# Optimization experiments

Measured on AMD Instinct MI355X. Metric: run time of the kernel, lower is better.

Reference implementation:

```python
import jax, jax.numpy as jnp
import numpy as np

N, E, NB = 50000, 100000, 6          # nodes, directed messages, max neighbors
NF, BF, H, DEPTH = 98, 6, 256, 6     # node feat, bond feat, hidden, depth
EF = NF + BF                          # edge_fdim: hmess = [fnode[src], bond_feats]


def setup_inputs() -> dict:
    key = jax.random.key(0)
    ks = jax.random.split(key, 12)
    s = lambda fan: np.float32(1.0 / np.sqrt(fan))
    return {
        "fnode": jax.random.normal(ks[0], (N, NF), jnp.float32),
        "fmess_idx": jax.random.randint(ks[1], (E, 2), 0, N),
        "fmess_feat": jax.random.normal(ks[2], (E, BF), jnp.float32),
        "agraph": jax.random.randint(ks[3], (N, NB), 0, E),
        "bgraph": jax.random.randint(ks[4], (E, NB), 0, E),
        "Wz": jax.random.normal(ks[5], (3, EF + H, H), jnp.float32) * s(EF + H),
        "bz": jnp.zeros((3, H), jnp.float32),
        "Wr": jax.random.normal(ks[6], (3, EF, H), jnp.float32) * s(EF),
        "Ur": jax.random.normal(ks[7], (3, H, H), jnp.float32) * s(H),
        "bur": jnp.zeros((3, H), jnp.float32),
        "Wh": jax.random.normal(ks[8], (3, EF + H, H), jnp.float32) * s(EF + H),
        "bh": jnp.zeros((3, H), jnp.float32),
        "Wo": jax.random.normal(ks[9], (3, NF + H, H), jnp.float32) * s(NF + H),
        "bo": jnp.zeros((3, H), jnp.float32),
    }


def _mpn(hnode, hmess, agraph, bgraph, Wz, bz, Wr, Ur, bur, Wh, bh, Wo, bo):
    # One MPNLayer: depth-unrolled message GRU over bgraph, then node readout via agraph.
    e_mask = jnp.ones((hmess.shape[0], 1), hmess.dtype).at[0, 0].set(0.0)  # msg 0 = padding
    r1 = hmess @ Wr  # W_r(fmess), loop-invariant  [E,H]

    def step(h, _):
        h_nei = h[bgraph]                                    # [E,NB,H] gather inbound msgs
        sum_h = h_nei.sum(axis=1)
        z = jax.nn.sigmoid(jnp.concatenate([hmess, sum_h], axis=1) @ Wz + bz)
        r = jax.nn.sigmoid(r1[:, None, :] + h_nei @ Ur + bur)  # [E,NB,H]
        sum_gh = (r * h_nei).sum(axis=1)
        pre_h = jnp.tanh(jnp.concatenate([hmess, sum_gh], axis=1) @ Wh + bh)
        return ((1.0 - z) * sum_h + z * pre_h) * e_mask, None

    h0 = jnp.zeros((hmess.shape[0], bz.shape[0]), hmess.dtype)
    h, _ = jax.lax.scan(step, h0, None, length=DEPTH)
    nei = h[agraph].sum(axis=1)                              # [N,H]
    node_h = jax.nn.relu(jnp.concatenate([hnode, nei], axis=1) @ Wo + bo)
    n_mask = jnp.ones((hnode.shape[0], 1), hnode.dtype).at[0, 0].set(0.0)  # node 0 = padding
    return node_h * n_mask


def reference(fnode, fmess_idx, fmess_feat, agraph, bgraph,
              Wz, bz, Wr, Ur, bur, Wh, bh, Wo, bo):
    # embed_graph: gather source-node features, concat with bond features
    hmess = jnp.concatenate([fnode[fmess_idx[:, 0]], fmess_feat], axis=1)  # [E,EF]
    run = jax.vmap(lambda a, b, c, d, e, f, g, hh, i: _mpn(
        fnode, hmess, agraph, bgraph, a, b, c, d, e, f, g, hh, i))
    qkv = run(Wz, bz, Wr, Ur, bur, Wh, bh, Wo, bo)           # [3,N,H]: Q/K/V encoders batched
    return (qkv[0], qkv[1], qkv[2])
```

## Files before the change

kernel.cpp:

```cpp
#include <hip/hip_runtime.h>


#define NE 100000
#define NEP 100032
#define NN 50000

typedef unsigned short u16;
typedef short short8 __attribute__((ext_vector_type(8)));
typedef float f32x4 __attribute__((ext_vector_type(4)));
typedef unsigned short u16x4 __attribute__((ext_vector_type(4)));

__device__ __forceinline__ float b2f(u16 u) {
  union { unsigned int i; float f; } v; v.i = ((unsigned int)u) << 16; return v.f;
}
__device__ __forceinline__ u16 f2b(float f) {
  union { float f; unsigned int i; } v; v.f = f;
  unsigned int b = v.i;
  b += 0x7FFFu + ((b >> 16) & 1u);
  return (u16)(b >> 16);
}
__device__ __forceinline__ unsigned cvtpk(float lo, float hi) {
  unsigned r;
  asm("v_cvt_pk_bf16_f32 %0, %1, %2" : "=v"(r) : "v"(lo), "v"(hi));
  return r;
}
__device__ __forceinline__ int swzB(int Q) { return Q ^ ((Q >> 4) & 7); }
__device__ __forceinline__ float sigm(float x) { return 1.0f / (1.0f + __expf(-x)); }
__device__ __forceinline__ float tanh_f(float x) { return 2.0f / (1.0f + __expf(-2.0f * x)) - 1.0f; }
__device__ __forceinline__ f32x4 mfma16(short8 a, short8 b, f32x4 c) {
  return __builtin_amdgcn_mfma_f32_16x16x32_bf16(a, b, c, 0, 0, 0);
}

__global__ void pack_wpre(const float* __restrict__ Wr, const float* __restrict__ Wz,
                          const float* __restrict__ Wh, u16* __restrict__ dst) {
  const int g = blockIdx.y;
  const int p = blockIdx.x * 256 + threadIdx.x;
  const int j = p & 7, l = (p >> 3) & 63, q = p >> 9;
  const int nb = q % 48, s = q / 48;
  const int k = 32 * s + 8 * (l >> 4) + j;
  const int n = 16 * nb + (l & 15);
  float v = 0.f;
  if (k < 104) {
    if (n < 256)      v = Wr[((size_t)g * 104 + k) * 256 + n];
    else if (n < 512) v = Wz[((size_t)g * 360 + k) * 256 + (n - 256)];
    else              v = Wh[((size_t)g * 360 + k) * 256 + (n - 512)];
  }
  dst[(size_t)g * 98304 + p] = f2b(v);
}

__global__ void pack_wgate(const float* __restrict__ Wz, const float* __restrict__ Wh,
                           u16* __restrict__ dst) {
  const int g = blockIdx.y;
  const int p = blockIdx.x * 256 + threadIdx.x;
  const int j = p & 7, l = (p >> 3) & 63, q = p >> 9;
  const int nb = q % 32, s = q / 32;
  const int k = 32 * s + 8 * (l >> 4) + j;
  const int n = 16 * nb + (l & 15);
  float v = (n < 256) ? Wz[((size_t)g * 360 + 104 + k) * 256 + n]
                      : Wh[((size_t)g * 360 + 104 + k) * 256 + (n - 256)];
  dst[(size_t)g * 131072 + p] = f2b(v);
}

__global__ void pack_ur(const float* __restrict__ Ur, u16* __restrict__ dst) {
  const int g = blockIdx.y;
  const int p = blockIdx.x * 256 + threadIdx.x;
  const int j = p & 7, l = (p >> 3) & 63, q = p >> 9;
  const int nb = q % 16, s = q / 16;
  const int k = 32 * s + 8 * (l >> 4) + j;
  const int n = 16 * nb + (l & 15);
  dst[(size_t)g * 65536 + p] = f2b(Ur[((size_t)g * 256 + k) * 256 + n]);
}

__global__ void pack_wo(const float* __restrict__ Wo, u16* __restrict__ dst) {
  const int g = blockIdx.y;
  const int p = blockIdx.x * 256 + threadIdx.x;
  const int j = p & 7, l = (p >> 3) & 63, q = p >> 9;
  const int nb = q % 16, s = q / 16;
  const int k = 32 * s + 8 * (l >> 4) + j;
  const int n = 16 * nb + (l & 15);
  float v = 0.f;
  if (k < 98)        v = Wo[((size_t)g * 354 + k) * 256 + n];
  else if (k >= 128) v = Wo[((size_t)g * 354 + (k - 30)) * 256 + n];
  dst[(size_t)g * 98304 + p] = f2b(v);
}

__global__ void embed_hmess_f(const float* __restrict__ fnode, const int* __restrict__ fmess_idx,
                              const float* __restrict__ fmess_feat, u16* __restrict__ hmF) {
  const int e = blockIdx.x * 2 + (threadIdx.x >> 7);
  const int c = threadIdx.x & 127;
  const int src = fmess_idx[e * 2];
  float v = 0.f;
  if (c < 98)       v = fnode[(size_t)src * 98 + c];
  else if (c < 104) v = fmess_feat[(size_t)e * 6 + (c - 98)];
  hmF[(size_t)(e >> 4) * 2048 + ((c >> 5) * 64 + (e & 15) + 16 * ((c >> 3) & 3)) * 8 + (c & 7)] = f2b(v);
}

__global__ void embed_fnode(const float* __restrict__ fnode, u16* __restrict__ fnp) {
  const int n = blockIdx.x * 2 + (threadIdx.x >> 7);
  const int c = threadIdx.x & 127;
  float v = (c < 98) ? fnode[(size_t)n * 98 + c] : 0.f;
  fnp[(size_t)n * 128 + c] = f2b(v);
}

__global__ __launch_bounds__(256)
void pre_gemm_t(const u16* __restrict__ hmF, const u16* __restrict__ Wpre,
                const float* __restrict__ bur, const float* __restrict__ bz,
                const float* __restrict__ bh, u16* __restrict__ r1b,
                u16* __restrict__ zpF, u16* __restrict__ hpF) {
  const int tid = threadIdx.x, wave = tid >> 6, lane = tid & 63;
  const int row0 = lane & 15, kq = lane >> 4;
  const int e0 = blockIdx.x * 32;
  const int cchunk = blockIdx.y;
  f32x4 acc[2][4];
#pragma unroll
  for (int i = 0; i < 2; ++i)
#pragma unroll
    for (int n = 0; n < 4; ++n) { acc[i][n][0]=0.f; acc[i][n][1]=0.f; acc[i][n][2]=0.f; acc[i][n][3]=0.f; }
#pragma unroll
  for (int kc = 0; kc < 4; ++kc) {
    short8 bf[2];
#pragma unroll
    for (int ef = 0; ef < 2; ++ef)
      bf[ef] = *(const short8*)(hmF + (size_t)((e0 >> 4) + ef) * 2048 + (size_t)(kc * 64 + lane) * 8);
#pragma unroll
    for (int nf = 0; nf < 4; ++nf) {
      const int nb = cchunk * 16 + wave * 4 + nf;
      short8 wf = *(const short8*)(Wpre + ((size_t)(kc * 48 + nb) * 64 + lane) * 8);
      acc[0][nf] = mfma16(wf, bf[0], acc[0][nf]);
      acc[1][nf] = mfma16(wf, bf[1], acc[1][nf]);
    }
  }
  const float* bias = (cchunk == 0) ? bur : (cchunk == 1 ? bz : bh);
  u16* dstF = (cchunk == 1) ? zpF : hpF;
#pragma unroll
  for (int ef = 0; ef < 2; ++ef)
#pragma unroll
    for (int nf = 0; nf < 4; ++nf) {
      const int n256 = wave * 64 + nf * 16 + kq * 4;
      const int e = e0 + ef * 16 + row0;
      u16x4 o;
#pragma unroll
      for (int v = 0; v < 4; ++v) o[v] = f2b(acc[ef][nf][v] + bias[n256 + v]);
      if (cchunk == 0) {
        *(u16x4*)(r1b + (size_t)e * 256 + n256) = o;
      } else {
        *(u16x4*)(dstF + ((size_t)((e0 >> 4) + ef) * 16 + (wave * 4 + nf)) * 256 + lane * 4) = o;
      }
    }
}

__global__ __launch_bounds__(512, 4)
void mpn_fused(const u16* __restrict__ HBin, u16* __restrict__ HBout,
               const u16* __restrict__ r1b, const int* __restrict__ bgraph,
               const u16* __restrict__ zpF, const u16* __restrict__ hpF,
               const u16* __restrict__ Wgate, const u16* __restrict__ Urp) {
  __shared__ __align__(16) u16 sF[32768];
  const int tid = threadIdx.x;
  const int wn = tid >> 6, lane = tid & 63;
  const int row0 = lane & 15, kq = lane >> 4;
  const int e0 = blockIdx.x * 64;

  {
    const int c0 = 4 * lane;
    const int Bc = (c0 >> 5) * 64 + 16 * ((c0 >> 3) & 3);
    const int sub = c0 & 7;
#pragma unroll 2
    for (int rr = 0; rr < 8; ++rr) {
      const int r = wn * 8 + rr;
      const int e = e0 + r;
      float sh[4] = {0.f, 0.f, 0.f, 0.f}, sg[4] = {0.f, 0.f, 0.f, 0.f};
      if (e < NE) {
        const u16x4 r1v = *(const u16x4*)(r1b + (size_t)e * 256 + c0);
        int idx[6];
#pragma unroll
        for (int k = 0; k < 6; ++k) idx[k] = bgraph[e * 6 + k];
        u16x4 hv[6], huv[6];
#pragma unroll
        for (int k = 0; k < 6; ++k) {
          const u16* rowp = HBin + (size_t)idx[k] * 512;
          hv[k]  = *(const u16x4*)(rowp + c0);
          huv[k] = *(const u16x4*)(rowp + 256 + c0);
        }
#pragma unroll
        for (int k = 0; k < 6; ++k)
#pragma unroll
          for (int j = 0; j < 4; ++j) {
            const float h  = b2f(hv[k][j]);
            const float rg = sigm(b2f(r1v[j]) + b2f(huv[k][j]));
            sh[j] += h;
            sg[j] += rg * h;
          }
      }
      const int Q = (r >> 4) * 512 + Bc + (r & 15);
      const int ao = swzB(Q) * 8 + sub;
      union { unsigned w[2]; u16x4 q; } p0, p1;
      p0.w[0] = cvtpk(sh[0], sh[1]); p0.w[1] = cvtpk(sh[2], sh[3]);
      p1.w[0] = cvtpk(sg[0], sg[1]); p1.w[1] = cvtpk(sg[2], sg[3]);
      *(u16x4*)(sF + ao) = p0.q;
      *(u16x4*)(sF + 16384 + ao) = p1.q;
    }
  }
  __syncthreads();

  f32x4 aZ[2][4], aH[2][4];
#pragma unroll
  for (int nf = 0; nf < 2; ++nf)
#pragma unroll
    for (int ef = 0; ef < 4; ++ef) {
      aZ[nf][ef][0]=0.f; aZ[nf][ef][1]=0.f; aZ[nf][ef][2]=0.f; aZ[nf][ef][3]=0.f;
      aH[nf][ef][0]=0.f; aH[nf][ef][1]=0.f; aH[nf][ef][2]=0.f; aH[nf][ef][3]=0.f;
    }
#pragma unroll
  for (int kc = 0; kc < 8; ++kc) {
    short8 wz0 = *(const short8*)(Wgate + ((size_t)(kc * 32 + wn * 2 + 0) * 64 + lane) * 8);
    short8 wz1 = *(const short8*)(Wgate + ((size_t)(kc * 32 + wn * 2 + 1) * 64 + lane) * 8);
    short8 wh0 = *(const short8*)(Wgate + ((size_t)(kc * 32 + 16 + wn * 2 + 0) * 64 + lane) * 8);
    short8 wh1 = *(const short8*)(Wgate + ((size_t)(kc * 32 + 16 + wn * 2 + 1) * 64 + lane) * 8);
#pragma unroll
    for (int ef = 0; ef < 4; ++ef) {
      const int ar = swzB(ef * 512 + kc * 64 + lane) * 8;
      short8 bsh = *(const short8*)(sF + ar);
      short8 bsg = *(const short8*)(sF + 16384 + ar);
      aZ[0][ef] = mfma16(wz0, bsh, aZ[0][ef]);
      aZ[1][ef] = mfma16(wz1, bsh, aZ[1][ef]);
      aH[0][ef] = mfma16(wh0, bsg, aH[0][ef]);
      aH[1][ef] = mfma16(wh1, bsg, aH[1][ef]);
    }
  }

  u16x4 hq[2][4];
#pragma unroll
  for (int nf = 0; nf < 2; ++nf) {
    const int lp = row0 + 16 * (nf * 2 + (kq >> 1));
    const int jo = 4 * (kq & 1);
    const int nc = wn * 2 + nf;
#pragma unroll
    for (int ef = 0; ef < 4; ++ef) {
      const int ev = (e0 + ef * 16) < NE;
      const int e  = e0 + ef * 16 + row0;
      const int as = swzB(ef * 512 + wn * 64 + lp) * 8 + jo;
      const u16x4 shv = *(const u16x4*)(sF + as);
      const size_t tb = ((size_t)((e0 >> 4) + ef) * 16 + nc) * 256 + lane * 4;
      const u16x4 zp4 = *(const u16x4*)(zpF + tb);
      const u16x4 hp4 = *(const u16x4*)(hpF + tb);
      float hf[4];
#pragma unroll
      for (int v = 0; v < 4; ++v) {
        const float z  = sigm(b2f(zp4[v]) + aZ[nf][ef][v]);
        const float ph = tanh_f(b2f(hp4[v]) + aH[nf][ef][v]);
        float h = (1.0f - z) * b2f(shv[v]) + z * ph;
        if (e == 0 || !ev) h = 0.f;
        hf[v] = h;
      }
      union { unsigned w[2]; u16x4 q; } pk;
      pk.w[0] = cvtpk(hf[0], hf[1]);
      pk.w[1] = cvtpk(hf[2], hf[3]);
      hq[nf][ef] = pk.q;
    }
  }
  __syncthreads();

#pragma unroll
  for (int nf = 0; nf < 2; ++nf) {
    const int lp = row0 + 16 * (nf * 2 + (kq >> 1));
    const int jo = 4 * (kq & 1);
#pragma unroll
    for (int ef = 0; ef < 4; ++ef) {
      const int as = swzB(ef * 512 + wn * 64 + lp) * 8 + jo;
      *(u16x4*)(sF + 16384 + as) = hq[nf][ef];
    }
  }
  __syncthreads();

  f32x4 aU[2][4];
#pragma unroll
  for (int nf = 0; nf < 2; ++nf)
#pragma unroll
    for (int ef = 0; ef < 4; ++ef) { aU[nf][ef][0]=0.f; aU[nf][ef][1]=0.f; aU[nf][ef][2]=0.f; aU[nf][ef][3]=0.f; }
#pragma unroll
  for (int kc = 0; kc < 8; ++kc) {
    short8 u0 = *(const short8*)(Urp + ((size_t)(kc * 16 + wn * 2 + 0) * 64 + lane) * 8);
    short8 u1 = *(const short8*)(Urp + ((size_t)(kc * 16 + wn * 2 + 1) * 64 + lane) * 8);
#pragma unroll
    for (int ef = 0; ef < 4; ++ef) {
      const int ar = swzB(ef * 512 + kc * 64 + lane) * 8;
      short8 hb = *(const short8*)(sF + 16384 + ar);
      aU[0][ef] = mfma16(u0, hb, aU[0][ef]);
      aU[1][ef] = mfma16(u1, hb, aU[1][ef]);
    }
  }

  {
    const int r = tid >> 3;
    const int e = e0 + r;
    if (e < NE) {
#pragma unroll
      for (int it = 0; it < 4; ++it) {
        const int c = (tid & 7) * 8 + it * 64;
        const int Qn = (r >> 4) * 512 + (c >> 5) * 64 + (r & 15) + 16 * ((c >> 3) & 3);
        const short8 val = *(const short8*)(sF + 16384 + swzB(Qn) * 8);
        *(short8*)(HBout + (size_t)e * 512 + c) = val;
      }
    }
  }
#pragma unroll
  for (int nf = 0; nf < 2; ++nf) {
    const int lp = row0 + 16 * (nf * 2 + (kq >> 1));
    const int jo = 4 * (kq & 1);
#pragma unroll
    for (int ef = 0; ef < 4; ++ef) {
      const int as = swzB(ef * 512 + wn * 64 + lp) * 8 + jo;
      union { unsigned w[2]; u16x4 q; } pk;
      pk.w[0] = cvtpk(aU[nf][ef][0], aU[nf][ef][1]);
      pk.w[1] = cvtpk(aU[nf][ef][2], aU[nf][ef][3]);
      *(u16x4*)(sF + as) = pk.q;
    }
  }
  __syncthreads();

  {
    const int r = tid >> 3;
    const int e = e0 + r;
    if (e < NE) {
#pragma unroll
      for (int it = 0; it < 4; ++it) {
        const int c = (tid & 7) * 8 + it * 64;
        const int Qn = (r >> 4) * 512 + (c >> 5) * 64 + (r & 15) + 16 * ((c >> 3) & 3);
        const short8 val = *(const short8*)(sF + swzB(Qn) * 8);
        *(short8*)(HBout + (size_t)e * 512 + 256 + c) = val;
      }
    }
  }
}

__global__ __launch_bounds__(512, 4)
void step0(u16* __restrict__ HB, const u16* __restrict__ zpF, const u16* __restrict__ hpF,
           const u16* __restrict__ Urp) {
  __shared__ __align__(16) u16 sHn[16384];
  const int tid = threadIdx.x;
  const int wn = tid >> 6, lane = tid & 63;
  const int row0 = lane & 15, kq = lane >> 4;
  const int e0 = blockIdx.x * 64;

#pragma unroll
  for (int nf = 0; nf < 2; ++nf) {
    const int lp = row0 + 16 * (nf * 2 + (kq >> 1));
    const int jo = 4 * (kq & 1);
    const int nc = wn * 2 + nf;
#pragma unroll
    for (int ef = 0; ef < 4; ++ef) {
      const int ev = (e0 + ef * 16) < NE;
      const int e  = e0 + ef * 16 + row0;
      const size_t tb = ((size_t)((e0 >> 4) + ef) * 16 + nc) * 256 + lane * 4;
      const u16x4 zp4 = *(const u16x4*)(zpF + tb);
      const u16x4 hp4 = *(const u16x4*)(hpF + tb);
      u16x4 hq;
#pragma unroll
      for (int v = 0; v < 4; ++v) {
        float hf = sigm(b2f(zp4[v])) * tanh_f(b2f(hp4[v]));
        if (e == 0 || !ev) hf = 0.f;
        hq[v] = f2b(hf);
      }
      *(u16x4*)(sHn + (size_t)ef * 4096 + (size_t)(wn * 64 + lp) * 8 + jo) = hq;
    }
  }
  __syncthreads();

  f32x4 aU[2][4];
#pragma unroll
  for (int nf = 0; nf < 2; ++nf)
#pragma unroll
    for (int ef = 0; ef < 4; ++ef) { aU[nf][ef][0]=0.f; aU[nf][ef][1]=0.f; aU[nf][ef][2]=0.f; aU[nf][ef][3]=0.f; }
#pragma unroll
  for (int kc = 0; kc < 8; ++kc) {
    short8 u0 = *(const short8*)(Urp + ((size_t)(kc * 16 + wn * 2 + 0) * 64 + lane) * 8);
    short8 u1 = *(const short8*)(Urp + ((size_t)(kc * 16 + wn * 2 + 1) * 64 + lane) * 8);
#pragma unroll
    for (int ef = 0; ef < 4; ++ef) {
      short8 hb = *(const short8*)(sHn + (size_t)ef * 4096 + (size_t)(kc * 64 + lane) * 8);
      aU[0][ef] = mfma16(u0, hb, aU[0][ef]);
      aU[1][ef] = mfma16(u1, hb, aU[1][ef]);
    }
  }
  {
    const int r = tid >> 3;
    const int e = e0 + r;
    if (e < NE) {
#pragma unroll
      for (int it = 0; it < 4; ++it) {
        const int c = (tid & 7) * 8 + it * 64;
        const short8 val = *(const short8*)(sHn + (size_t)(r >> 4) * 4096 +
                           (size_t)(((c >> 5) * 64 + (r & 15) + 16 * ((c >> 3) & 3)) * 8));
        *(short8*)(HB + (size_t)e * 512 + c) = val;
      }
    }
  }
  __syncthreads();
#pragma unroll
  for (int nf = 0; nf < 2; ++nf) {
    const int lp = row0 + 16 * (nf * 2 + (kq >> 1));
    const int jo = 4 * (kq & 1);
#pragma unroll
    for (int ef = 0; ef < 4; ++ef) {
      u16x4 uq;
#pragma unroll
      for (int v = 0; v < 4; ++v) uq[v] = f2b(aU[nf][ef][v]);
      *(u16x4*)(sHn + (size_t)ef * 4096 + (size_t)(wn * 64 + lp) * 8 + jo) = uq;
    }
  }
  __syncthreads();
  {
    const int r = tid >> 3;
    const int e = e0 + r;
    if (e < NE) {
#pragma unroll
      for (int it = 0; it < 4; ++it) {
        const int c = (tid & 7) * 8 + it * 64;
        const short8 val = *(const short8*)(sHn + (size_t)(r >> 4) * 4096 +
                           (size_t)(((c >> 5) * 64 + (r & 15) + 16 * ((c >> 3) & 3)) * 8));
        *(short8*)(HB + (size_t)e * 512 + 256 + c) = val;
      }
    }
  }
}

__global__ __launch_bounds__(256)
void readout(const u16* __restrict__ HB, const u16* __restrict__ fnp,
             const int* __restrict__ agraph, const u16* __restrict__ Wop,
             const float* __restrict__ bo, float* __restrict__ out) {
  __shared__ __align__(16) u16 sN[32][264];
  const int tid = threadIdx.x, wave = tid >> 6, lane = tid & 63;
  const int n0 = blockIdx.x * 32;
  const int row0 = lane & 15, kq = lane >> 4;

#pragma unroll 2
  for (int rr = 0; rr < 8; ++rr) {
    const int r = wave * 8 + rr;
    const int n = n0 + r;
    float s4[4] = {0.f, 0.f, 0.f, 0.f};
    if (n < NN) {
#pragma unroll
      for (int k = 0; k < 6; ++k) {
        const int idx = agraph[n * 6 + k];
        const u16x4 hv = *(const u16x4*)(HB + (size_t)idx * 512 + 4 * lane);
#pragma unroll
        for (int j = 0; j < 4; ++j) s4[j] += b2f(hv[j]);
      }
    }
#pragma unroll
    for (int j = 0; j < 4; ++j) sN[r][4 * lane + j] = f2b(s4[j]);
  }
  __syncthreads();

  f32x4 acc[2][4];
#pragma unroll
  for (int i = 0; i < 2; ++i)
#pragma unroll
    for (int n = 0; n < 4; ++n) { acc[i][n][0]=0.f; acc[i][n][1]=0.f; acc[i][n][2]=0.f; acc[i][n][3]=0.f; }
  const int ra = min(n0 + row0, NN - 1);
  const int rb = min(n0 + 16 + row0, NN - 1);
#pragma unroll
  for (int s = 0; s < 12; ++s) {
    short8 a0, a1;
    if (s < 4) {
      a0 = *(const short8*)(fnp + (size_t)ra * 128 + s * 32 + kq * 8);
      a1 = *(const short8*)(fnp + (size_t)rb * 128 + s * 32 + kq * 8);
    } else {
      a0 = *(const short8*)&sN[row0][(s - 4) * 32 + kq * 8];
      a1 = *(const short8*)&sN[row0 + 16][(s - 4) * 32 + kq * 8];
    }
#pragma unroll
    for (int ni = 0; ni < 4; ++ni) {
      short8 b = *(const short8*)(Wop + ((size_t)(s * 16 + wave * 4 + ni) * 64 + lane) * 8);
      acc[0][ni] = mfma16(a0, b, acc[0][ni]);
      acc[1][ni] = mfma16(a1, b, acc[1][ni]);
    }
  }
#pragma unroll
  for (int mi = 0; mi < 2; ++mi)
#pragma unroll
    for (int ni = 0; ni < 4; ++ni)
#pragma unroll
      for (int v = 0; v < 4; ++v) {
        const int m = mi * 16 + kq * 4 + v;
        const int col = wave * 64 + ni * 16 + row0;
        const int n = n0 + m;
        if (n < NN) {
          float val = fmaxf(acc[mi][ni][v] + bo[col], 0.f);
          if (n == 0) val = 0.f;
          out[(size_t)n * 256 + col] = val;
        }
      }
}

extern "C" void kernel_launch(void* const* d_in, const int* in_sizes, int n_in,
                              void* d_out, int out_size, void* d_ws, size_t ws_size,
                              hipStream_t stream) {
  const float* fnode      = (const float*)d_in[0];
  const int*   fmess_idx  = (const int*)d_in[1];
  const float* fmess_feat = (const float*)d_in[2];
  const int*   agraph     = (const int*)d_in[3];
  const int*   bgraph     = (const int*)d_in[4];
  const float* Wz         = (const float*)d_in[5];
  const float* bz         = (const float*)d_in[6];
  const float* Wr         = (const float*)d_in[7];
  const float* Ur         = (const float*)d_in[8];
  const float* bur        = (const float*)d_in[9];
  const float* Wh         = (const float*)d_in[10];
  const float* bh         = (const float*)d_in[11];
  const float* Wo         = (const float*)d_in[12];
  const float* bo         = (const float*)d_in[13];
  float* out = (float*)d_out;

  char* ws = (char*)d_ws;
  size_t off = 0;
  auto carve = [&](size_t bytes) -> char* {
    char* p = ws + off;
    off += (bytes + 511) & ~(size_t)511;
    return p;
  };
  u16* HB0  = (u16*)carve((size_t)NEP * 512 * 2);
  u16* HB1  = (u16*)carve((size_t)NEP * 512 * 2);
  u16* r1b  = (u16*)carve((size_t)NEP * 256 * 2);
  u16* zpF  = (u16*)carve((size_t)NEP * 256 * 2);
  u16* hpF  = (u16*)carve((size_t)NEP * 256 * 2);
  u16* hmF  = (u16*)carve((size_t)NEP * 128 * 2);
  u16* fnp  = (u16*)carve((size_t)NN * 128 * 2);
  u16* wpre = (u16*)carve((size_t)3 * 98304 * 2);
  u16* wgate= (u16*)carve((size_t)3 * 131072 * 2);
  u16* urp  = (u16*)carve((size_t)3 * 65536 * 2);
  u16* wop  = (u16*)carve((size_t)3 * 98304 * 2);
  if (off > ws_size) return;

  pack_wpre <<<dim3(384, 3), 256, 0, stream>>>(Wr, Wz, Wh, wpre);
  pack_wgate<<<dim3(512, 3), 256, 0, stream>>>(Wz, Wh, wgate);
  pack_ur   <<<dim3(256, 3), 256, 0, stream>>>(Ur, urp);
  pack_wo   <<<dim3(384, 3), 256, 0, stream>>>(Wo, wop);
  embed_hmess_f<<<NE / 2, 256, 0, stream>>>(fnode, fmess_idx, fmess_feat, hmF);
  embed_fnode<<<NN / 2, 256, 0, stream>>>(fnode, fnp);

  for (int g = 0; g < 3; ++g) {
    pre_gemm_t<<<dim3(NEP / 32, 3), 256, 0, stream>>>(
        hmF, wpre + (size_t)g * 98304, bur + g * 256, bz + g * 256, bh + g * 256,
        r1b, zpF, hpF);
    const u16* wgate_g = wgate + (size_t)g * 131072;
    const u16* urp_g   = urp + (size_t)g * 65536;
    step0<<<NEP / 64, 512, 0, stream>>>(HB0, zpF, hpF, urp_g);
    u16* bufs[2] = {HB0, HB1};
    int cur = 0;
    for (int d = 1; d < 6; ++d) {
      mpn_fused<<<NEP / 64, 512, 0, stream>>>(bufs[cur], bufs[1 - cur], r1b, bgraph,
                                              zpF, hpF, wgate_g, urp_g);
      cur ^= 1;
    }
    readout<<<(NN + 31) / 32, 256, 0, stream>>>(
        bufs[cur], fnp, agraph, wop + (size_t)g * 98304, bo + g * 256, out + (size_t)g * NN * 256);
  }
}
```

Baseline: 3.546 ms.

## Halve mpn_fused edge tile to 32 rows, drop swizzle and bounds checks

Shrinks the per-block edge tile of the fused message kernel from 64 to 32 rows, halving shared memory to 32 KB and raising the launch-bounds occupancy target to 8 blocks. The LDS swizzle is removed in favor of a plain fragment layout. Since NE is divisible by 32, the grid covers exactly NE edges and the e<NE checks are dropped. The aim is more resident waves to hide the latency of the random bgraph gathers, at the cost of reloading the Wgate/Ur weights in twice as many blocks and possible LDS bank conflicts without the swizzle.

```diff
diff --git a/kernel.cpp b/kernel.cpp
--- a/kernel.cpp
+++ b/kernel.cpp
@@ -24,7 +24,6 @@
   asm("v_cvt_pk_bf16_f32 %0, %1, %2" : "=v"(r) : "v"(lo), "v"(hi));
   return r;
 }
-__device__ __forceinline__ int swzB(int Q) { return Q ^ ((Q >> 4) & 7); }
 __device__ __forceinline__ float sigm(float x) { return 1.0f / (1.0f + __expf(-x)); }
 __device__ __forceinline__ float tanh_f(float x) { return 2.0f / (1.0f + __expf(-2.0f * x)) - 1.0f; }
 __device__ __forceinline__ f32x4 mfma16(short8 a, short8 b, f32x4 c) {
@@ -149,64 +148,60 @@
     }
 }
 
-__global__ __launch_bounds__(512, 4)
+__global__ __launch_bounds__(512, 8)
 void mpn_fused(const u16* __restrict__ HBin, u16* __restrict__ HBout,
                const u16* __restrict__ r1b, const int* __restrict__ bgraph,
                const u16* __restrict__ zpF, const u16* __restrict__ hpF,
                const u16* __restrict__ Wgate, const u16* __restrict__ Urp) {
-  __shared__ __align__(16) u16 sF[32768];
+  __shared__ __align__(16) u16 sF[16384];
   const int tid = threadIdx.x;
   const int wn = tid >> 6, lane = tid & 63;
   const int row0 = lane & 15, kq = lane >> 4;
-  const int e0 = blockIdx.x * 64;
+  const int e0 = blockIdx.x * 32;
 
   {
     const int c0 = 4 * lane;
-    const int Bc = (c0 >> 5) * 64 + 16 * ((c0 >> 3) & 3);
-    const int sub = c0 & 7;
+    const int offc = ((c0 >> 5) * 64 + 16 * ((c0 >> 3) & 3)) * 8 + (c0 & 7);
 #pragma unroll 2
-    for (int rr = 0; rr < 8; ++rr) {
-      const int r = wn * 8 + rr;
+    for (int rr = 0; rr < 4; ++rr) {
+      const int r = wn * 4 + rr;
       const int e = e0 + r;
+      const u16x4 r1v = *(const u16x4*)(r1b + (size_t)e * 256 + c0);
+      int idx[6];
+#pragma unroll
+      for (int k = 0; k < 6; ++k) idx[k] = bgraph[e * 6 + k];
+      u16x4 hv[6], huv[6];
+#pragma unroll
+      for (int k = 0; k < 6; ++k) {
+        const u16* rowp = HBin + (size_t)idx[k] * 512;
+        hv[k]  = *(const u16x4*)(rowp + c0);
+        huv[k] = *(const u16x4*)(rowp + 256 + c0);
+      }
       float sh[4] = {0.f, 0.f, 0.f, 0.f}, sg[4] = {0.f, 0.f, 0.f, 0.f};
-      if (e < NE) {
-        const u16x4 r1v = *(const u16x4*)(r1b + (size_t)e * 256 + c0);
-        int idx[6];
-#pragma unroll
-        for (int k = 0; k < 6; ++k) idx[k] = bgraph[e * 6 + k];
-        u16x4 hv[6], huv[6];
-#pragma unroll
-        for (int k = 0; k < 6; ++k) {
-          const u16* rowp = HBin + (size_t)idx[k] * 512;
-          hv[k]  = *(const u16x4*)(rowp + c0);
-          huv[k] = *(const u16x4*)(rowp + 256 + c0);
+#pragma unroll
+      for (int k = 0; k < 6; ++k)
+#pragma unroll
+        for (int j = 0; j < 4; ++j) {
+          const float h  = b2f(hv[k][j]);
+          const float rg = sigm(b2f(r1v[j]) + b2f(huv[k][j]));
+          sh[j] += h;
+          sg[j] += rg * h;
         }
-#pragma unroll
-        for (int k = 0; k < 6; ++k)
-#pragma unroll
-          for (int j = 0; j < 4; ++j) {
-            const float h  = b2f(hv[k][j]);
-            const float rg = sigm(b2f(r1v[j]) + b2f(huv[k][j]));
-            sh[j] += h;
-            sg[j] += rg * h;
-          }
-      }
-      const int Q = (r >> 4) * 512 + Bc + (r & 15);
-      const int ao = swzB(Q) * 8 + sub;
+      const int off = (r >> 4) * 4096 + offc + (r & 15) * 8;
       union { unsigned w[2]; u16x4 q; } p0, p1;
       p0.w[0] = cvtpk(sh[0], sh[1]); p0.w[1] = cvtpk(sh[2], sh[3]);
       p1.w[0] = cvtpk(sg[0], sg[1]); p1.w[1] = cvtpk(sg[2], sg[3]);
-      *(u16x4*)(sF + ao) = p0.q;
-      *(u16x4*)(sF + 16384 + ao) = p1.q;
-    }
-  }
-  __syncthreads();
-
-  f32x4 aZ[2][4], aH[2][4];
+      *(u16x4*)(sF + off) = p0.q;
+      *(u16x4*)(sF + 8192 + off) = p1.q;
+    }
+  }
+  __syncthreads();
+
+  f32x4 aZ[2][2], aH[2][2];
 #pragma unroll
   for (int nf = 0; nf < 2; ++nf)
 #pragma unroll
-    for (int ef = 0; ef < 4; ++ef) {
+    for (int ef = 0; ef < 2; ++ef) {
       aZ[nf][ef][0]=0.f; aZ[nf][ef][1]=0.f; aZ[nf][ef][2]=0.f; aZ[nf][ef][3]=0.f;
       aH[nf][ef][0]=0.f; aH[nf][ef][1]=0.f; aH[nf][ef][2]=0.f; aH[nf][ef][3]=0.f;
     }
@@ -217,10 +212,9 @@
     short8 wh0 = *(const short8*)(Wgate + ((size_t)(kc * 32 + 16 + wn * 2 + 0) * 64 + lane) * 8);
     short8 wh1 = *(const short8*)(Wgate + ((size_t)(kc * 32 + 16 + wn * 2 + 1) * 64 + lane) * 8);
 #pragma unroll
-    for (int ef = 0; ef < 4; ++ef) {
-      const int ar = swzB(ef * 512 + kc * 64 + lane) * 8;
-      short8 bsh = *(const short8*)(sF + ar);
-      short8 bsg = *(const short8*)(sF + 16384 + ar);
+    for (int ef = 0; ef < 2; ++ef) {
+      short8 bsh = *(const short8*)(sF + ef * 4096 + (kc * 64 + lane) * 8);
+      short8 bsg = *(const short8*)(sF + 8192 + ef * 4096 + (kc * 64 + lane) * 8);
       aZ[0][ef] = mfma16(wz0, bsh, aZ[0][ef]);
       aZ[1][ef] = mfma16(wz1, bsh, aZ[1][ef]);
       aH[0][ef] = mfma16(wh0, bsg, aH[0][ef]);
@@ -228,17 +222,16 @@
     }
   }
 
-  u16x4 hq[2][4];
+  u16x4 hq[2][2];
 #pragma unroll
   for (int nf = 0; nf < 2; ++nf) {
     const int lp = row0 + 16 * (nf * 2 + (kq >> 1));
     const int jo = 4 * (kq & 1);
     const int nc = wn * 2 + nf;
 #pragma unroll
-    for (int ef = 0; ef < 4; ++ef) {
-      const int ev = (e0 + ef * 16) < NE;
-      const int e  = e0 + ef * 16 + row0;
-      const int as = swzB(ef * 512 + wn * 64 + lp) * 8 + jo;
+    for (int ef = 0; ef < 2; ++ef) {
+      const int e = e0 + ef * 16 + row0;
+      const int as = ef * 4096 + (wn * 64 + lp) * 8 + jo;
       const u16x4 shv = *(const u16x4*)(sF + as);
       const size_t tb = ((size_t)((e0 >> 4) + ef) * 16 + nc) * 256 + lane * 4;
       const u16x4 zp4 = *(const u16x4*)(zpF + tb);
@@ -249,7 +242,7 @@
         const float z  = sigm(b2f(zp4[v]) + aZ[nf][ef][v]);
         const float ph = tanh_f(b2f(hp4[v]) + aH[nf][ef][v]);
         float h = (1.0f - z) * b2f(shv[v]) + z * ph;
-        if (e == 0 || !ev) h = 0.f;
+        if (e == 0) h = 0.f;
         hf[v] = h;
       }
       union { unsigned w[2]; u16x4 q; } pk;
@@ -265,42 +258,37 @@
     const int lp = row0 + 16 * (nf * 2 + (kq >> 1));
     const int jo = 4 * (kq & 1);
 #pragma unroll
-    for (int ef = 0; ef < 4; ++ef) {
-      const int as = swzB(ef * 512 + wn * 64 + lp) * 8 + jo;
-      *(u16x4*)(sF + 16384 + as) = hq[nf][ef];
-    }
-  }
-  __syncthreads();
-
-  f32x4 aU[2][4];
+    for (int ef = 0; ef < 2; ++ef)
+      *(u16x4*)(sF + 8192 + ef * 4096 + (wn * 64 + lp) * 8 + jo) = hq[nf][ef];
+  }
+  __syncthreads();
+
+  f32x4 aU[2][2];
 #pragma unroll
   for (int nf = 0; nf < 2; ++nf)
 #pragma unroll
-    for (int ef = 0; ef < 4; ++ef) { aU[nf][ef][0]=0.f; aU[nf][ef][1]=0.f; aU[nf][ef][2]=0.f; aU[nf][ef][3]=0.f; }
+    for (int ef = 0; ef < 2; ++ef) { aU[nf][ef][0]=0.f; aU[nf][ef][1]=0.f; aU[nf][ef][2]=0.f; aU[nf][ef][3]=0.f; }
 #pragma unroll
   for (int kc = 0; kc < 8; ++kc) {
     short8 u0 = *(const short8*)(Urp + ((size_t)(kc * 16 + wn * 2 + 0) * 64 + lane) * 8);
     short8 u1 = *(const short8*)(Urp + ((size_t)(kc * 16 + wn * 2 + 1) * 64 + lane) * 8);
 #pragma unroll
-    for (int ef = 0; ef < 4; ++ef) {
-      const int ar = swzB(ef * 512 + kc * 64 + lane) * 8;
-      short8 hb = *(const short8*)(sF + 16384 + ar);
+    for (int ef = 0; ef < 2; ++ef) {
+      short8 hb = *(const short8*)(sF + 8192 + ef * 4096 + (kc * 64 + lane) * 8);
       aU[0][ef] = mfma16(u0, hb, aU[0][ef]);
       aU[1][ef] = mfma16(u1, hb, aU[1][ef]);
     }
   }
 
   {
-    const int r = tid >> 3;
+    const int r = tid >> 4;
     const int e = e0 + r;
-    if (e < NE) {
-#pragma unroll
-      for (int it = 0; it < 4; ++it) {
-        const int c = (tid & 7) * 8 + it * 64;
-        const int Qn = (r >> 4) * 512 + (c >> 5) * 64 + (r & 15) + 16 * ((c >> 3) & 3);
-        const short8 val = *(const short8*)(sF + 16384 + swzB(Qn) * 8);
-        *(short8*)(HBout + (size_t)e * 512 + c) = val;
-      }
+#pragma unroll
+    for (int it = 0; it < 2; ++it) {
+      const int c = (tid & 15) * 8 + it * 128;
+      const short8 val = *(const short8*)(sF + 8192 + (r >> 4) * 4096 +
+                         (((c >> 5) * 64 + (r & 15) + 16 * ((c >> 3) & 3)) * 8));
+      *(short8*)(HBout + (size_t)e * 512 + c) = val;
     }
   }
 #pragma unroll
@@ -308,27 +296,24 @@
     const int lp = row0 + 16 * (nf * 2 + (kq >> 1));
     const int jo = 4 * (kq & 1);
 #pragma unroll
-    for (int ef = 0; ef < 4; ++ef) {
-      const int as = swzB(ef * 512 + wn * 64 + lp) * 8 + jo;
+    for (int ef = 0; ef < 2; ++ef) {
       union { unsigned w[2]; u16x4 q; } pk;
       pk.w[0] = cvtpk(aU[nf][ef][0], aU[nf][ef][1]);
       pk.w[1] = cvtpk(aU[nf][ef][2], aU[nf][ef][3]);
-      *(u16x4*)(sF + as) = pk.q;
+      *(u16x4*)(sF + ef * 4096 + (wn * 64 + lp) * 8 + jo) = pk.q;
     }
   }
   __syncthreads();
 
   {
-    const int r = tid >> 3;
+    const int r = tid >> 4;
     const int e = e0 + r;
-    if (e < NE) {
-#pragma unroll
-      for (int it = 0; it < 4; ++it) {
-        const int c = (tid & 7) * 8 + it * 64;
-        const int Qn = (r >> 4) * 512 + (c >> 5) * 64 + (r & 15) + 16 * ((c >> 3) & 3);
-        const short8 val = *(const short8*)(sF + swzB(Qn) * 8);
-        *(short8*)(HBout + (size_t)e * 512 + 256 + c) = val;
-      }
+#pragma unroll
+    for (int it = 0; it < 2; ++it) {
+      const int c = (tid & 15) * 8 + it * 128;
+      const short8 val = *(const short8*)(sF + (r >> 4) * 4096 +
+                         (((c >> 5) * 64 + (r & 15) + 16 * ((c >> 3) & 3)) * 8));
+      *(short8*)(HBout + (size_t)e * 512 + 256 + c) = val;
     }
   }
 }
@@ -549,8 +534,8 @@
     u16* bufs[2] = {HB0, HB1};
     int cur = 0;
     for (int d = 1; d < 6; ++d) {
-      mpn_fused<<<NEP / 64, 512, 0, stream>>>(bufs[cur], bufs[1 - cur], r1b, bgraph,
-                                              zpF, hpF, wgate_g, urp_g);
+      mpn_fused<<<NE / 32, 512, 0, stream>>>(bufs[cur], bufs[1 - cur], r1b, bgraph,
+                                             zpF, hpF, wgate_g, urp_g);
       cur ^= 1;
     }
     readout<<<(NN + 31) / 32, 256, 0, stream>>>(
```

Result: slower. 3.699 ms (+4.3%).
